# Kernel tuning notes

Hardware: AMD Instinct MI355X
Metric: run time of the kernel (lower is better)

The kernel has to match this reference:

```python
import jax, jax.numpy as jnp
import numpy as np

N, E, K, G = 50000, 800000, 3, 64
F_IN, F_HID, F_OUT, N_CLS = 128, 192, 128, 10
LAMBDA_MAX = 2.0  # PyG ChebConv default when lambda_max is None and normalization='sym'


def setup_inputs() -> dict:
    key = jax.random.key(0)
    ks = jax.random.split(key, 12)
    x = jax.random.normal(ks[0], (N, F_IN), dtype=jnp.float32)
    edge_index = jax.random.randint(ks[1], (2, E), 0, N)
    batch = jnp.sort(jax.random.randint(ks[2], (N,), 0, G))

    def mkW(k, fi, fo):
        return jax.random.normal(k, (K, fi, fo), dtype=jnp.float32) / np.float32(np.sqrt(K * fi))

    W1 = mkW(ks[3], F_IN, F_HID)
    b1 = jax.random.normal(ks[4], (F_HID,), dtype=jnp.float32) * 0.01
    W2 = mkW(ks[5], F_HID, F_HID)
    b2 = jax.random.normal(ks[6], (F_HID,), dtype=jnp.float32) * 0.01
    W3 = mkW(ks[7], F_HID, F_OUT)
    b3 = jax.random.normal(ks[8], (F_OUT,), dtype=jnp.float32) * 0.01
    fc_w = jax.random.normal(ks[9], (F_OUT, N_CLS), dtype=jnp.float32) / np.float32(np.sqrt(F_OUT))
    fc_b = jax.random.normal(ks[10], (N_CLS,), dtype=jnp.float32) * 0.01
    return {"x": x, "edge_index": edge_index, "batch": batch,
            "W1": W1, "b1": b1, "W2": W2, "b2": b2, "W3": W3, "b3": b3,
            "fc_w": fc_w, "fc_b": fc_b}


def reference(x, edge_index, batch, W1, b1, W2, b2, W3, b3, fc_w, fc_b):
    row, col = edge_index[0], edge_index[1]
    # symmetric scaled Laplacian: L_hat = (2/lmax) * (I - D^-1/2 A D^-1/2) - I
    deg = jax.ops.segment_sum(jnp.ones((E,), x.dtype), row, num_segments=N)
    dis = jnp.where(deg > 0, jax.lax.rsqrt(jnp.maximum(deg, 1e-12)), 0.0)
    scale = 2.0 / LAMBDA_MAX
    w_edge = (-scale) * dis[row] * dis[col]  # off-diagonal entries of L_hat
    diag_w = scale - 1.0                      # diagonal entries (0 when lmax=2)

    def prop(h):  # h: [N, F] -> L_hat @ h
        return jax.ops.segment_sum(w_edge[:, None] * h[col], row, num_segments=N) + diag_w * h

    def cheb_conv(h, W, b):
        Tx0 = h
        out = Tx0 @ W[0]
        Tx1 = prop(Tx0)
        out = out + Tx1 @ W[1]
        for k in range(2, K):
            Tx2 = 2.0 * prop(Tx1) - Tx0
            out = out + Tx2 @ W[k]
            Tx0, Tx1 = Tx1, Tx2
        return out + b

    h = cheb_conv(x, W1, b1)
    h = cheb_conv(h, W2, b2)
    h = cheb_conv(h, W3, b3)

    # global mean pool over graphs
    sums = jax.ops.segment_sum(h, batch, num_segments=G)
    cnts = jax.ops.segment_sum(jnp.ones((N,), h.dtype), batch, num_segments=G)
    pooled = sums / jnp.maximum(cnts, 1.0)[:, None]  # [G, F_OUT]

    logits = pooled @ fc_w + fc_b
    return jax.nn.log_softmax(logits, axis=1)
```

## Files before the change

kernel.cpp:

```cpp
#include <hip/hip_runtime.h>
#include <math.h>

#define N_NODES 50000
#define N_EDGES 800000
#define N_GRAPHS 64
#define F_INN 128
#define F_HID 192
#define F_OUTT 128
#define N_CLS 10

typedef short short8 __attribute__((ext_vector_type(8)));
typedef float f32x4 __attribute__((ext_vector_type(4)));

static __device__ inline unsigned short f2bf(float f) {
    unsigned int u = __float_as_uint(f);
    unsigned int r = (u + 0x7FFFu + ((u >> 16) & 1u)) >> 16;
    return (unsigned short)r;
}
static __device__ inline float bf2f(unsigned short h) {
    return __uint_as_float(((unsigned int)h) << 16);
}

__global__ void k_deg(const int* __restrict__ row, int* __restrict__ cnt,
                      int* __restrict__ rank) {
    int e = blockIdx.x * 256 + threadIdx.x;
    if (e < N_EDGES) rank[e] = atomicAdd(&cnt[row[e]], 1);
}

__global__ void k_scan1(const int* __restrict__ cnt, int* __restrict__ rp,
                        int* __restrict__ part, float* __restrict__ dis) {
    __shared__ int s[256];
    int base = blockIdx.x * 512;
    int i0 = base + 2 * threadIdx.x;
    int v0 = (i0 < N_NODES) ? cnt[i0] : 0;
    int v1 = (i0 + 1 < N_NODES) ? cnt[i0 + 1] : 0;
    if (i0 < N_NODES) dis[i0] = v0 > 0 ? rsqrtf((float)v0) : 0.f;
    if (i0 + 1 < N_NODES) dis[i0 + 1] = v1 > 0 ? rsqrtf((float)v1) : 0.f;
    int tsum = v0 + v1;
    s[threadIdx.x] = tsum;
    __syncthreads();
    for (int off = 1; off < 256; off <<= 1) {
        int val = (threadIdx.x >= off) ? s[threadIdx.x - off] : 0;
        __syncthreads();
        s[threadIdx.x] += val;
        __syncthreads();
    }
    int excl = s[threadIdx.x] - tsum;
    if (i0 < N_NODES) rp[i0] = excl;
    if (i0 + 1 < N_NODES) rp[i0 + 1] = excl + v0;
    if (threadIdx.x == 255) part[blockIdx.x] = s[255];
}

__global__ void k_scan3(int* __restrict__ rp, const int* __restrict__ part,
                        int nb) {
    __shared__ int s[128];
    int t = threadIdx.x;
    int b = blockIdx.x;
    if (t < 128) s[t] = (t < b && t < nb) ? part[t] : 0;
    __syncthreads();
    for (int off = 64; off > 0; off >>= 1) {
        if (t < off) s[t] += s[t + off];
        __syncthreads();
    }
    int add = s[0];
    int i0 = b * 512 + 2 * t;
    if (i0 < N_NODES) rp[i0] += add;
    if (i0 + 1 < N_NODES) rp[i0 + 1] += add;
    if (b == 0 && t == 0) rp[N_NODES] = N_EDGES;
}

__global__ void k_scatter(const int* __restrict__ row, const int* __restrict__ col,
                          const float* __restrict__ dis, const int* __restrict__ rp,
                          const int* __restrict__ rank, int2* __restrict__ cw) {
    int e = blockIdx.x * 256 + threadIdx.x;
    if (e < N_EDGES) {
        int r = row[e], c = col[e];
        int pos = rp[r] + rank[e];
        int2 v;
        v.x = c;
        v.y = __float_as_int(-dis[r] * dis[c]);
        cw[pos] = v;
    }
}

#define NX (N_NODES * F_INN)
#define NW1 (3 * 128 * 192)
#define NW2 (3 * 192 * 192)
#define NW3 (3 * 192 * 128)
#define NPS (3 * N_GRAPHS * F_HID)
__global__ void k_convAll(const float* __restrict__ x, const float* __restrict__ W1,
                          const float* __restrict__ W2, const float* __restrict__ W3,
                          unsigned short* __restrict__ xb,
                          unsigned short* __restrict__ Wt1,
                          unsigned short* __restrict__ Wt2,
                          unsigned short* __restrict__ Wt3,
                          int* __restrict__ cnt, float* __restrict__ psum) {
    int idx = blockIdx.x * 256 + threadIdx.x;
    if (idx < NX) {
        xb[idx] = f2bf(x[idx]);
        return;
    }
    idx -= NX;
    if (idx < NW1) {
        int per = 128 * 192;
        int j = idx / per, r = idx - j * per;
        int k = r / 192, n = r - k * 192;
        float v = (j == 0) ? (W1[idx] - W1[idx + 2 * per])
                           : (j == 2 ? 2.f * W1[idx] : W1[idx]);
        Wt1[j * per + n * 128 + k] = f2bf(v);
        return;
    }
    idx -= NW1;
    if (idx < NW2) {
        int per = 192 * 192;
        int j = idx / per, r = idx - j * per;
        int k = r / 192, n = r - k * 192;
        float v = (j == 0) ? (W2[idx] - W2[idx + 2 * per])
                           : (j == 2 ? 2.f * W2[idx] : W2[idx]);
        Wt2[j * per + n * 192 + k] = f2bf(v);
        return;
    }
    idx -= NW2;
    if (idx < NW3) {
        int per = 192 * 128;
        int j = idx / per, r = idx - j * per;
        int k = r / 128, n = r - k * 128;
        float v = (j == 0) ? (W3[idx] - W3[idx + 2 * per])
                           : (j == 2 ? 2.f * W3[idx] : W3[idx]);
        Wt3[j * per + n * 192 + k] = f2bf(v);
        return;
    }
    idx -= NW3;
    if (idx < N_NODES) {
        cnt[idx] = 0;
        return;
    }
    idx -= N_NODES;
    if (idx < NPS) psum[idx] = 0.f;
}

template <int F>
__global__ void k_spmv(const int* __restrict__ rp, const int2* __restrict__ cw,
                       const unsigned short* __restrict__ h,
                       unsigned short* __restrict__ y) {
    constexpr bool EX = (F > 128);
    constexpr int FU = F / 2;
    int wave = threadIdx.x >> 6;
    int lane = threadIdx.x & 63;
    int r = blockIdx.x * 4 + wave;
    if (r >= N_NODES) return;
    int e0 = __builtin_amdgcn_readfirstlane(rp[r]);
    int e1 = __builtin_amdgcn_readfirstlane(rp[r + 1]);
    const unsigned int* hu = (const unsigned int*)h;
    float a0 = 0.f, a1 = 0.f, a2 = 0.f;
    int e = e0;
    for (; e + 8 <= e1; e += 8) {
        int colv[8];
        float wv[8];
#pragma unroll
        for (int u = 0; u < 8; u++) {
            int2 p = cw[e + u];
            colv[u] = __builtin_amdgcn_readfirstlane(p.x);
            wv[u] = __uint_as_float(__builtin_amdgcn_readfirstlane(p.y));
        }
        unsigned int g[8];
        unsigned short s[8];
#pragma unroll
        for (int u = 0; u < 8; u++) {
            g[u] = hu[colv[u] * FU + lane];
            if constexpr (EX) s[u] = h[colv[u] * F + 128 + lane];
        }
#pragma unroll
        for (int u = 0; u < 8; u++) {
            a0 += wv[u] * bf2f((unsigned short)g[u]);
            a1 += wv[u] * bf2f((unsigned short)(g[u] >> 16));
            if constexpr (EX) a2 += wv[u] * bf2f(s[u]);
        }
    }
    for (; e + 4 <= e1; e += 4) {
        int colv[4];
        float wv[4];
#pragma unroll
        for (int u = 0; u < 4; u++) {
            int2 p = cw[e + u];
            colv[u] = __builtin_amdgcn_readfirstlane(p.x);
            wv[u] = __uint_as_float(__builtin_amdgcn_readfirstlane(p.y));
        }
        unsigned int g[4];
        unsigned short s[4];
#pragma unroll
        for (int u = 0; u < 4; u++) {
            g[u] = hu[colv[u] * FU + lane];
            if constexpr (EX) s[u] = h[colv[u] * F + 128 + lane];
        }
#pragma unroll
        for (int u = 0; u < 4; u++) {
            a0 += wv[u] * bf2f((unsigned short)g[u]);
            a1 += wv[u] * bf2f((unsigned short)(g[u] >> 16));
            if constexpr (EX) a2 += wv[u] * bf2f(s[u]);
        }
    }
    for (; e < e1; e++) {
        int2 p = cw[e];
        int c = __builtin_amdgcn_readfirstlane(p.x);
        float w = __uint_as_float(__builtin_amdgcn_readfirstlane(p.y));
        unsigned int g = hu[c * FU + lane];
        a0 += w * bf2f((unsigned short)g);
        a1 += w * bf2f((unsigned short)(g >> 16));
        if constexpr (EX) a2 += w * bf2f(h[c * F + 128 + lane]);
    }
    ((unsigned int*)y)[r * FU + lane] =
        (unsigned int)f2bf(a0) | ((unsigned int)f2bf(a1) << 16);
    if constexpr (EX) y[r * F + 128 + lane] = f2bf(a2);
}

template <int Fin, int Fout>
__global__ __launch_bounds__(256) void k_gemm3(
    const unsigned short* __restrict__ A0, const unsigned short* __restrict__ A1,
    const unsigned short* __restrict__ A2, const unsigned short* __restrict__ Wt,
    const float* __restrict__ bias, unsigned short* __restrict__ C) {
    constexpr int NF = Fout / 16;
    constexpr int BP = Fout / 64;
    __shared__ unsigned short As[128 * 40];
    __shared__ unsigned short Bs[Fout * 40];
    int t = threadIdx.x;
    int w = t >> 6;
    int lane = t & 63;
    int ml = lane & 15;
    int quad = lane >> 4;
    int mBase = blockIdx.x * 128;
    constexpr int per = Fin * Fout;

    f32x4 acc[2][NF];
#pragma unroll
    for (int i = 0; i < 2; i++)
#pragma unroll
        for (int jn = 0; jn < NF; jn++) acc[i][jn] = (f32x4){0.f, 0.f, 0.f, 0.f};

    int srow = t >> 2;
    int schunk = t & 3;
    constexpr int nChunks = (3 * Fin) >> 5;

    for (int ch = 0; ch < nChunks; ch++) {
        int kg = ch << 5;
        int j = kg / Fin;
        int kk = kg - j * Fin;
        const unsigned short* Aj = (j == 0) ? A0 : (j == 1) ? A1 : A2;
        if (ch > 0) __syncthreads();
#pragma unroll
        for (int pass = 0; pass < 2; pass++) {
            int row = srow + pass * 64;
            int gm = mBase + row;
            uint4 v = {0u, 0u, 0u, 0u};
            if (gm < N_NODES)
                v = *(const uint4*)(Aj + (size_t)gm * Fin + kk + schunk * 8);
            *(uint4*)&As[row * 40 + schunk * 8] = v;
        }
#pragma unroll
        for (int pass = 0; pass < BP; pass++) {
            int row = srow + pass * 64;
            const unsigned short* src =
                Wt + (size_t)j * per + (size_t)row * Fin + kk + schunk * 8;
            *(uint4*)&Bs[row * 40 + schunk * 8] = *(const uint4*)src;
        }
        __syncthreads();

        short8 afr[2];
#pragma unroll
        for (int i = 0; i < 2; i++)
            afr[i] = *(const short8*)&As[(w * 32 + i * 16 + ml) * 40 + quad * 8];
#pragma unroll
        for (int jn = 0; jn < NF; jn++) {
            short8 bfr = *(const short8*)&Bs[(jn * 16 + ml) * 40 + quad * 8];
#pragma unroll
            for (int i = 0; i < 2; i++)
                acc[i][jn] = __builtin_amdgcn_mfma_f32_16x16x32_bf16(
                    afr[i], bfr, acc[i][jn], 0, 0, 0);
        }
    }

    float biasv[NF];
#pragma unroll
    for (int jn = 0; jn < NF; jn++) biasv[jn] = bias[jn * 16 + ml];

#pragma unroll
    for (int i = 0; i < 2; i++) {
#pragma unroll
        for (int r = 0; r < 4; r++) {
            int m = mBase + w * 32 + i * 16 + quad * 4 + r;
            if (m < N_NODES) {
                unsigned short* cp = C + (size_t)m * Fout + ml;
#pragma unroll
                for (int jn = 0; jn < NF; jn++)
                    cp[jn * 16] = f2bf(acc[i][jn][r] + biasv[jn]);
            }
        }
    }
}

__global__ __launch_bounds__(256) void k_pool3(
    const unsigned short* __restrict__ x3, const unsigned short* __restrict__ g1,
    const unsigned short* __restrict__ g2, const int* __restrict__ batch,
    float* __restrict__ psum) {
    int wave = threadIdx.x >> 6;
    int lane = threadIdx.x & 63;
    int r0 = blockIdx.x * 256;
    int r1 = r0 + 256;
    if (r1 > N_NODES) r1 = N_NODES;
    const unsigned int* xu = (const unsigned int*)x3;
    const unsigned int* au = (const unsigned int*)g1;
    const unsigned int* bu = (const unsigned int*)g2;
    float x0 = 0.f, x1 = 0.f, x2 = 0.f;
    float a0 = 0.f, a1 = 0.f, a2 = 0.f;
    float b0 = 0.f, b1 = 0.f, b2 = 0.f;
    int curg = -1;
    for (int r = r0 + wave; r < r1; r += 4) {
        int g = __builtin_amdgcn_readfirstlane(batch[r]);
        if (g != curg) {
            if (curg >= 0) {
                float* p0 = psum + curg * 192;
                atomicAdd(&p0[2 * lane], x0);
                atomicAdd(&p0[2 * lane + 1], x1);
                atomicAdd(&p0[128 + lane], x2);
                float* p1 = p0 + N_GRAPHS * 192;
                atomicAdd(&p1[2 * lane], a0);
                atomicAdd(&p1[2 * lane + 1], a1);
                atomicAdd(&p1[128 + lane], a2);
                float* p2 = p1 + N_GRAPHS * 192;
                atomicAdd(&p2[2 * lane], b0);
                atomicAdd(&p2[2 * lane + 1], b1);
                atomicAdd(&p2[128 + lane], b2);
                x0 = x1 = x2 = a0 = a1 = a2 = b0 = b1 = b2 = 0.f;
            }
            curg = g;
        }
        unsigned int vx = xu[(size_t)r * 96 + lane];
        unsigned int va = au[(size_t)r * 96 + lane];
        unsigned int vb = bu[(size_t)r * 96 + lane];
        unsigned short sx = x3[(size_t)r * 192 + 128 + lane];
        unsigned short sa = g1[(size_t)r * 192 + 128 + lane];
        unsigned short sb = g2[(size_t)r * 192 + 128 + lane];
        x0 += bf2f((unsigned short)vx);
        x1 += bf2f((unsigned short)(vx >> 16));
        x2 += bf2f(sx);
        a0 += bf2f((unsigned short)va);
        a1 += bf2f((unsigned short)(va >> 16));
        a2 += bf2f(sa);
        b0 += bf2f((unsigned short)vb);
        b1 += bf2f((unsigned short)(vb >> 16));
        b2 += bf2f(sb);
    }
    if (curg >= 0) {
        float* p0 = psum + curg * 192;
        atomicAdd(&p0[2 * lane], x0);
        atomicAdd(&p0[2 * lane + 1], x1);
        atomicAdd(&p0[128 + lane], x2);
        float* p1 = p0 + N_GRAPHS * 192;
        atomicAdd(&p1[2 * lane], a0);
        atomicAdd(&p1[2 * lane + 1], a1);
        atomicAdd(&p1[128 + lane], a2);
        float* p2 = p1 + N_GRAPHS * 192;
        atomicAdd(&p2[2 * lane], b0);
        atomicAdd(&p2[2 * lane + 1], b1);
        atomicAdd(&p2[128 + lane], b2);
    }
}

__global__ __launch_bounds__(128) void k_head2(
    const float* __restrict__ psum,
    const unsigned short* __restrict__ Wt3, const float* __restrict__ b3,
    const int* __restrict__ batch, const float* __restrict__ fcw,
    const float* __restrict__ fcb, float* __restrict__ out) {
    int g = blockIdx.x;
    int t = threadIdx.x;
    __shared__ float ps[3 * 192];
    __shared__ float m3[F_OUTT];
    __shared__ float sl[N_CLS];
    for (int i = t; i < 192; i += 128) {
        ps[i] = psum[g * 192 + i];
        ps[192 + i] = psum[N_GRAPHS * 192 + g * 192 + i];
        ps[384 + i] = psum[2 * N_GRAPHS * 192 + g * 192 + i];
    }
    __syncthreads();
    int a = 0, b = N_NODES;
    while (a < b) { int m = (a + b) >> 1; if (batch[m] < g) a = m + 1; else b = m; }
    int lo = a;
    a = lo; b = N_NODES;
    while (a < b) { int m = (a + b) >> 1; if (batch[m] < g + 1) a = m + 1; else b = m; }
    float inv = 1.f / fmaxf((float)(a - lo), 1.f);
    constexpr int per = 192 * F_OUTT;
    float accv = 0.f;
    const unsigned short* wp = Wt3 + (size_t)t * 192;
#pragma unroll 4
    for (int k = 0; k < 192; k += 8) {
        short8 v0 = *(const short8*)(wp + k);
        short8 v1 = *(const short8*)(wp + per + k);
        short8 v2 = *(const short8*)(wp + 2 * per + k);
#pragma unroll
        for (int j = 0; j < 8; j++)
            accv += ps[k + j] * bf2f((unsigned short)v0[j]) +
                    ps[192 + k + j] * bf2f((unsigned short)v1[j]) +
                    ps[384 + k + j] * bf2f((unsigned short)v2[j]);
    }
    m3[t] = accv * inv + b3[t];
    __syncthreads();
    if (t < N_CLS) {
        float l = fcb[t];
        for (int n = 0; n < F_OUTT; n++) l += m3[n] * fcw[n * N_CLS + t];
        sl[t] = l;
    }
    __syncthreads();
    if (t < N_CLS) {
        float mx = -1e30f;
        for (int i = 0; i < N_CLS; i++) mx = fmaxf(mx, sl[i]);
        float s = 0.f;
        for (int i = 0; i < N_CLS; i++) s += expf(sl[i] - mx);
        out[g * N_CLS + t] = sl[t] - mx - logf(s);
    }
}

extern "C" void kernel_launch(void* const* d_in, const int* in_sizes, int n_in,
                              void* d_out, int out_size, void* d_ws, size_t ws_size,
                              hipStream_t stream) {
    const float* x = (const float*)d_in[0];
    const int* ei = (const int*)d_in[1];
    const int* batch = (const int*)d_in[2];
    const float* W1 = (const float*)d_in[3];
    const float* b1 = (const float*)d_in[4];
    const float* W2 = (const float*)d_in[5];
    const float* b2 = (const float*)d_in[6];
    const float* W3 = (const float*)d_in[7];
    const float* b3 = (const float*)d_in[8];
    const float* fcw = (const float*)d_in[9];
    const float* fcb = (const float*)d_in[10];
    float* out = (float*)d_out;
    const int* row = ei;
    const int* col = ei + N_EDGES;

    char* p = (char*)d_ws;
    auto carve = [&](size_t bytes) {
        char* q = p;
        p += (bytes + 255) & ~(size_t)255;
        return q;
    };
    int* cnt = (int*)carve(N_NODES * 4);
    int* rank = (int*)carve((size_t)N_EDGES * 4);
    float* dis = (float*)carve(N_NODES * 4);
    int* rp = (int*)carve((N_NODES + 1) * 4);
    int* part = (int*)carve(128 * 4);
    int2* cw = (int2*)carve((size_t)N_EDGES * 8);
    unsigned short* xb = (unsigned short*)carve((size_t)N_NODES * F_INN * 2);
    size_t hbytes = (size_t)N_NODES * 192 * 2;
    unsigned short* bufA = (unsigned short*)carve(hbytes);
    unsigned short* bufB = (unsigned short*)carve(hbytes);
    unsigned short* bufC = (unsigned short*)carve(hbytes);
    unsigned short* bufD = (unsigned short*)carve(hbytes);
    unsigned short* Wt1 = (unsigned short*)carve(NW1 * 2);
    unsigned short* Wt2 = (unsigned short*)carve(NW2 * 2);
    unsigned short* Wt3 = (unsigned short*)carve(NW3 * 2);
    float* psum = (float*)carve(NPS * 4);

    {
        int tot = NX + NW1 + NW2 + NW3 + N_NODES + NPS;
        k_convAll<<<(tot + 255) / 256, 256, 0, stream>>>(x, W1, W2, W3, xb, Wt1, Wt2,
                                                         Wt3, cnt, psum);
    }

    k_deg<<<(N_EDGES + 255) / 256, 256, 0, stream>>>(row, cnt, rank);
    int nb = (N_NODES + 511) / 512;
    k_scan1<<<nb, 256, 0, stream>>>(cnt, rp, part, dis);
    k_scan3<<<nb, 256, 0, stream>>>(rp, part, nb);
    k_scatter<<<(N_EDGES + 255) / 256, 256, 0, stream>>>(row, col, dis, rp, rank, cw);

    const int spmvGrid = (N_NODES + 3) / 4;
    const int gemmGrid = (N_NODES + 127) / 128;

    k_spmv<128><<<spmvGrid, 256, 0, stream>>>(rp, cw, xb, bufB);
    k_spmv<128><<<spmvGrid, 256, 0, stream>>>(rp, cw, bufB, bufC);
    k_gemm3<128, 192><<<gemmGrid, 256, 0, stream>>>(xb, bufB, bufC, Wt1, b1, bufA);
    k_spmv<192><<<spmvGrid, 256, 0, stream>>>(rp, cw, bufA, bufB);
    k_spmv<192><<<spmvGrid, 256, 0, stream>>>(rp, cw, bufB, bufC);
    k_gemm3<192, 192><<<gemmGrid, 256, 0, stream>>>(bufA, bufB, bufC, Wt2, b2, bufD);
    k_spmv<192><<<spmvGrid, 256, 0, stream>>>(rp, cw, bufD, bufB);
    k_spmv<192><<<spmvGrid, 256, 0, stream>>>(rp, cw, bufB, bufC);
    k_pool3<<<(N_NODES + 255) / 256, 256, 0, stream>>>(bufD, bufB, bufC, batch, psum);

    k_head2<<<N_GRAPHS, 128, 0, stream>>>(psum, Wt3, b3, batch, fcw, fcb, out);
}
```

Baseline: 477.2 us.

## Fuse final SpMV into graph pooling via per-edge graph IDs

The last layer's second propagation (L·Tx1) is only needed for its per-graph mean, so it is no longer materialized. Instead, the pooled sum is computed directly over edges: each edge's weighted neighbor row is accumulated into the pool slot of its source node's graph, using a new per-edge graph-id byte array written in the scatter kernel. This skips writing and rereading a full N×192 buffer and removes one SpMV launch. In exchange it adds an edge-ordered gather pass, an extra byte array, and atomics whenever a wave crosses a graph boundary.

```diff
diff --git a/kernel.cpp b/kernel.cpp
--- a/kernel.cpp
+++ b/kernel.cpp
@@ -71,7 +71,8 @@
 
 __global__ void k_scatter(const int* __restrict__ row, const int* __restrict__ col,
                           const float* __restrict__ dis, const int* __restrict__ rp,
-                          const int* __restrict__ rank, int2* __restrict__ cw) {
+                          const int* __restrict__ rank, const int* __restrict__ batch,
+                          int2* __restrict__ cw, unsigned char* __restrict__ ge) {
     int e = blockIdx.x * 256 + threadIdx.x;
     if (e < N_EDGES) {
         int r = row[e], c = col[e];
@@ -80,6 +81,7 @@
         v.x = c;
         v.y = __float_as_int(-dis[r] * dis[c]);
         cw[pos] = v;
+        ge[pos] = (unsigned char)batch[r];
     }
 }
 
@@ -298,51 +300,43 @@
     }
 }
 
-__global__ __launch_bounds__(256) void k_pool3(
+__global__ __launch_bounds__(256) void k_gpoolS(
     const unsigned short* __restrict__ x3, const unsigned short* __restrict__ g1,
-    const unsigned short* __restrict__ g2, const int* __restrict__ batch,
-    float* __restrict__ psum) {
+    const int* __restrict__ batch, float* __restrict__ psum) {
     int wave = threadIdx.x >> 6;
     int lane = threadIdx.x & 63;
-    int r0 = blockIdx.x * 256;
-    int r1 = r0 + 256;
-    if (r1 > N_NODES) r1 = N_NODES;
-    const unsigned int* xu = (const unsigned int*)x3;
-    const unsigned int* au = (const unsigned int*)g1;
-    const unsigned int* bu = (const unsigned int*)g2;
-    float x0 = 0.f, x1 = 0.f, x2 = 0.f;
-    float a0 = 0.f, a1 = 0.f, a2 = 0.f;
-    float b0 = 0.f, b1 = 0.f, b2 = 0.f;
-    int curg = -1;
-    for (int r = r0 + wave; r < r1; r += 4) {
-        int g = __builtin_amdgcn_readfirstlane(batch[r]);
-        if (g != curg) {
-            if (curg >= 0) {
-                float* p0 = psum + curg * 192;
-                atomicAdd(&p0[2 * lane], x0);
-                atomicAdd(&p0[2 * lane + 1], x1);
-                atomicAdd(&p0[128 + lane], x2);
-                float* p1 = p0 + N_GRAPHS * 192;
-                atomicAdd(&p1[2 * lane], a0);
-                atomicAdd(&p1[2 * lane + 1], a1);
-                atomicAdd(&p1[128 + lane], a2);
-                float* p2 = p1 + N_GRAPHS * 192;
-                atomicAdd(&p2[2 * lane], b0);
-                atomicAdd(&p2[2 * lane + 1], b1);
-                atomicAdd(&p2[128 + lane], b2);
-                x0 = x1 = x2 = a0 = a1 = a2 = b0 = b1 = b2 = 0.f;
-            }
-            curg = g;
-        }
-        unsigned int vx = xu[(size_t)r * 96 + lane];
-        unsigned int va = au[(size_t)r * 96 + lane];
-        unsigned int vb = bu[(size_t)r * 96 + lane];
-        unsigned short sx = x3[(size_t)r * 192 + 128 + lane];
-        unsigned short sa = g1[(size_t)r * 192 + 128 + lane];
-        unsigned short sb = g2[(size_t)r * 192 + 128 + lane];
-        x0 += bf2f((unsigned short)vx);
-        x1 += bf2f((unsigned short)(vx >> 16));
-        x2 += bf2f(sx);
+    int w0 = blockIdx.x * 64 + wave * 16;
+    if (w0 >= N_NODES) return;
+    int n = N_NODES - w0;
+    if (n > 16) n = 16;
+    int bv = 0;
+    if (lane < 16 && w0 + lane < N_NODES) bv = batch[w0 + lane];
+    const unsigned int* au = (const unsigned int*)x3;
+    const unsigned int* bu = (const unsigned int*)g1;
+    float a0 = 0.f, a1 = 0.f, a2 = 0.f, b0 = 0.f, b1 = 0.f, b2 = 0.f;
+    int cur = __shfl(bv, 0);
+    auto flush = [&](int g) {
+        float* p0 = psum + (size_t)g * 192;
+        atomicAdd(&p0[2 * lane], a0);
+        atomicAdd(&p0[2 * lane + 1], a1);
+        atomicAdd(&p0[128 + lane], a2);
+        float* p1 = p0 + (size_t)N_GRAPHS * 192;
+        atomicAdd(&p1[2 * lane], b0);
+        atomicAdd(&p1[2 * lane + 1], b1);
+        atomicAdd(&p1[128 + lane], b2);
+    };
+    for (int i = 0; i < n; i++) {
+        int g = __shfl(bv, i);
+        if (g != cur) {
+            flush(cur);
+            a0 = a1 = a2 = b0 = b1 = b2 = 0.f;
+            cur = g;
+        }
+        size_t r = (size_t)(w0 + i);
+        unsigned int va = au[r * 96 + lane];
+        unsigned int vb = bu[r * 96 + lane];
+        unsigned short sa = x3[r * 192 + 128 + lane];
+        unsigned short sb = g1[r * 192 + 128 + lane];
         a0 += bf2f((unsigned short)va);
         a1 += bf2f((unsigned short)(va >> 16));
         a2 += bf2f(sa);
@@ -350,20 +344,75 @@
         b1 += bf2f((unsigned short)(vb >> 16));
         b2 += bf2f(sb);
     }
-    if (curg >= 0) {
-        float* p0 = psum + curg * 192;
-        atomicAdd(&p0[2 * lane], x0);
-        atomicAdd(&p0[2 * lane + 1], x1);
-        atomicAdd(&p0[128 + lane], x2);
-        float* p1 = p0 + N_GRAPHS * 192;
-        atomicAdd(&p1[2 * lane], a0);
-        atomicAdd(&p1[2 * lane + 1], a1);
-        atomicAdd(&p1[128 + lane], a2);
-        float* p2 = p1 + N_GRAPHS * 192;
-        atomicAdd(&p2[2 * lane], b0);
-        atomicAdd(&p2[2 * lane + 1], b1);
-        atomicAdd(&p2[128 + lane], b2);
-    }
+    flush(cur);
+}
+
+__global__ void k_gpool2(const int2* __restrict__ cw,
+                         const unsigned char* __restrict__ ge,
+                         const unsigned short* __restrict__ h,
+                         float* __restrict__ psum2) {
+    int wave = threadIdx.x >> 6;
+    int lane = threadIdx.x & 63;
+    int wid = blockIdx.x * 4 + wave;
+    if (wid >= N_EDGES / 256) return;
+    int eBeg = wid * 256;
+    int eEnd = eBeg + 256;
+    const unsigned int* hu = (const unsigned int*)h;
+    float a0 = 0.f, a1 = 0.f, a2 = 0.f;
+    int cur = __builtin_amdgcn_readfirstlane((int)ge[eBeg]);
+    auto flush = [&](int g) {
+        float* p = psum2 + (size_t)g * 192;
+        atomicAdd(&p[2 * lane], a0);
+        atomicAdd(&p[2 * lane + 1], a1);
+        atomicAdd(&p[128 + lane], a2);
+    };
+    for (int e = eBeg; e < eEnd; e += 8) {
+        uint2 gw = *(const uint2*)(ge + e);
+        unsigned int lo = __builtin_amdgcn_readfirstlane(gw.x);
+        unsigned int hi = __builtin_amdgcn_readfirstlane(gw.y);
+        unsigned int rep = 0x01010101u * (unsigned int)cur;
+        if (lo == rep && hi == rep) {
+            int colv[8];
+            float wv[8];
+#pragma unroll
+            for (int u = 0; u < 8; u++) {
+                int2 p = cw[e + u];
+                colv[u] = __builtin_amdgcn_readfirstlane(p.x);
+                wv[u] = __uint_as_float(__builtin_amdgcn_readfirstlane(p.y));
+            }
+            unsigned int g[8];
+            unsigned short s[8];
+#pragma unroll
+            for (int u = 0; u < 8; u++) {
+                g[u] = hu[colv[u] * 96 + lane];
+                s[u] = h[colv[u] * 192 + 128 + lane];
+            }
+#pragma unroll
+            for (int u = 0; u < 8; u++) {
+                a0 += wv[u] * bf2f((unsigned short)g[u]);
+                a1 += wv[u] * bf2f((unsigned short)(g[u] >> 16));
+                a2 += wv[u] * bf2f(s[u]);
+            }
+        } else {
+            for (int u = 0; u < 8; u++) {
+                unsigned int word = (u < 4) ? lo : hi;
+                int g = (int)((word >> (8 * (u & 3))) & 0xFFu);
+                if (g != cur) {
+                    flush(cur);
+                    a0 = a1 = a2 = 0.f;
+                    cur = g;
+                }
+                int2 p = cw[e + u];
+                int c = __builtin_amdgcn_readfirstlane(p.x);
+                float w = __uint_as_float(__builtin_amdgcn_readfirstlane(p.y));
+                unsigned int gv = hu[c * 96 + lane];
+                a0 += w * bf2f((unsigned short)gv);
+                a1 += w * bf2f((unsigned short)(gv >> 16));
+                a2 += w * bf2f(h[c * 192 + 128 + lane]);
+            }
+        }
+    }
+    flush(cur);
 }
 
 __global__ __launch_bounds__(128) void k_head2(
@@ -449,6 +498,7 @@
     int* rp = (int*)carve((N_NODES + 1) * 4);
     int* part = (int*)carve(128 * 4);
     int2* cw = (int2*)carve((size_t)N_EDGES * 8);
+    unsigned char* ge = (unsigned char*)carve((size_t)N_EDGES);
     unsigned short* xb = (unsigned short*)carve((size_t)N_NODES * F_INN * 2);
     size_t hbytes = (size_t)N_NODES * 192 * 2;
     unsigned short* bufA = (unsigned short*)carve(hbytes);
@@ -470,7 +520,8 @@
     int nb = (N_NODES + 511) / 512;
     k_scan1<<<nb, 256, 0, stream>>>(cnt, rp, part, dis);
     k_scan3<<<nb, 256, 0, stream>>>(rp, part, nb);
-    k_scatter<<<(N_EDGES + 255) / 256, 256, 0, stream>>>(row, col, dis, rp, rank, cw);
+    k_scatter<<<(N_EDGES + 255) / 256, 256, 0, stream>>>(row, col, dis, rp, rank,
+                                                         batch, cw, ge);
 
     const int spmvGrid = (N_NODES + 3) / 4;
     const int gemmGrid = (N_NODES + 127) / 128;
@@ -482,8 +533,9 @@
     k_spmv<192><<<spmvGrid, 256, 0, stream>>>(rp, cw, bufB, bufC);
     k_gemm3<192, 192><<<gemmGrid, 256, 0, stream>>>(bufA, bufB, bufC, Wt2, b2, bufD);
     k_spmv<192><<<spmvGrid, 256, 0, stream>>>(rp, cw, bufD, bufB);
-    k_spmv<192><<<spmvGrid, 256, 0, stream>>>(rp, cw, bufB, bufC);
-    k_pool3<<<(N_NODES + 255) / 256, 256, 0, stream>>>(bufD, bufB, bufC, batch, psum);
+    k_gpoolS<<<(N_NODES + 63) / 64, 256, 0, stream>>>(bufD, bufB, batch, psum);
+    k_gpool2<<<(N_EDGES / 256 + 3) / 4, 256, 0, stream>>>(
+        cw, ge, bufB, psum + 2 * N_GRAPHS * 192);
 
     k_head2<<<N_GRAPHS, 128, 0, stream>>>(psum, Wt3, b3, batch, fcw, fcb, out);
 }
```

New measurement: 481.4 us. Within noise of the previous version (+0.9%).
